# Kernel optimization log

Hardware: AMD Instinct MI355X
Metric: run time of the kernel (lower is better)

## Reference

```python
import jax, jax.numpy as jnp
import numpy as np

NODE = 100   # sensors per graph
BATCH = 64
DIM = 128    # embed dim == gnn out channels
IN_DIM = 5
TOPK = 30
INTER = 256  # out_layer hidden
EPS = 1e-5   # BatchNorm eps
SLOPE = 0.2  # leaky relu negative slope


def setup_inputs() -> dict:
    key = jax.random.key(0)
    ks = jax.random.split(key, 16)
    d = {
        "x": jax.random.normal(ks[0], (BATCH * NODE, IN_DIM), jnp.float32),
        "emb": jax.random.normal(ks[1], (NODE, DIM), jnp.float32) * 0.1,
        "w_lin": jax.random.normal(ks[2], (DIM, IN_DIM), jnp.float32) * (1.0 / np.sqrt(IN_DIM)),
        "att_i": jax.random.normal(ks[3], (DIM,), jnp.float32) * (1.0 / np.sqrt(DIM)),
        "att_j": jax.random.normal(ks[4], (DIM,), jnp.float32) * (1.0 / np.sqrt(DIM)),
        "att_em_i": jax.random.normal(ks[5], (DIM,), jnp.float32) * (1.0 / np.sqrt(DIM)),
        "att_em_j": jax.random.normal(ks[6], (DIM,), jnp.float32) * (1.0 / np.sqrt(DIM)),
        "g_bias": jax.random.normal(ks[7], (DIM,), jnp.float32) * 0.02,
        "bn1_g": jnp.ones((DIM,), jnp.float32),
        "bn1_b": jnp.zeros((DIM,), jnp.float32),
        "bn2_g": jnp.ones((DIM,), jnp.float32),
        "bn2_b": jnp.zeros((DIM,), jnp.float32),
        "bn3_g": jnp.ones((INTER,), jnp.float32),
        "bn3_b": jnp.zeros((INTER,), jnp.float32),
        "w1": jax.random.normal(ks[8], (INTER, DIM), jnp.float32) * (1.0 / np.sqrt(DIM)),
        "b1": jnp.zeros((INTER,), jnp.float32),
        "w2": jax.random.normal(ks[9], (1, INTER), jnp.float32) * (1.0 / np.sqrt(INTER)),
        "b2": jnp.zeros((1,), jnp.float32),
        "topk": TOPK,
    }
    return d


def _bn(z, g, b, axes):
    # BatchNorm1d in training mode: biased batch stats per channel (last axis)
    mu = z.mean(axes, keepdims=True)
    var = z.var(axes, keepdims=True)
    return (z - mu) / jnp.sqrt(var + EPS) * g + b


def reference(x, emb, w_lin, att_i, att_j, att_em_i, att_em_j, g_bias,
              bn1_g, bn1_b, bn2_g, bn2_b, bn3_g, bn3_b, w1, b1, w2, b2, topk):
    n, d = emb.shape
    nb = x.shape[0]            # batch*node rows
    bsz = nb // n

    # --- learned graph from cosine similarity of (detached) embeddings ---
    w = jax.lax.stop_gradient(emb)
    nrm = jnp.linalg.norm(w, axis=-1)
    cos = (w @ w.T) / (nrm[:, None] * nrm[None, :])
    _, idx = jax.lax.top_k(cos, topk)              # [n, k] neighbors j per target i
    src = idx.reshape(-1)                          # gated_j (source)
    dst = jnp.repeat(jnp.arange(n), topk)          # gated_i (target)
    off = (jnp.arange(bsz) * n)[:, None]
    src_b = (src[None, :] + off).reshape(-1)       # [bsz*n*k]
    dst_b = (dst[None, :] + off).reshape(-1)

    # --- GraphLayer: lin + gather + edge attention + segment softmax + scatter-add ---
    h = x @ w_lin.T                                # [nb, d]
    x_i = h[dst_b]
    x_j = h[src_b]
    emb_i = emb[dst_b % n]                         # all_embeddings repeated per batch
    emb_j = emb[src_b % n]
    alpha = x_i @ att_i + emb_i @ att_em_i + x_j @ att_j + emb_j @ att_em_j  # [E]
    alpha = jnp.where(alpha > 0, alpha, SLOPE * alpha)
    # segment softmax keyed by target node
    m = jax.ops.segment_max(alpha, dst_b, num_segments=nb)
    a = jnp.exp(alpha - m[dst_b])
    s = jax.ops.segment_sum(a, dst_b, num_segments=nb)
    attw = a / (s[dst_b] + 1e-16)
    agg = jax.ops.segment_sum(x_j * attw[:, None], dst_b, num_segments=nb) + g_bias

    # GNNLayer: BN + ReLU
    y = jax.nn.relu(_bn(agg, bn1_g, bn1_b, 0))     # [nb, d]

    # --- GDN head ---
    x3 = y.reshape(bsz, n, d) * emb[None]          # mul with node embeddings
    x3 = jax.nn.relu(_bn(x3, bn2_g, bn2_b, (0, 1)))
    # OutLayer: Linear -> BN -> ReLU -> Linear
    o = x3 @ w1.T + b1                             # [bsz, n, INTER]
    o = jax.nn.relu(_bn(o, bn3_g, bn3_b, (0, 1)))
    o = o @ w2.T + b2                              # [bsz, n, 1]
    return o.reshape(-1, 1)
```

## Files before the change

kernel.cpp:

```cpp
#include <hip/hip_runtime.h>

#define NODE 100
#define BATCH 64
#define DIM 128
#define IN_DIM 5
#define TOPK 30
#define INTER 256
#define NB (BATCH*NODE)
#define EPS 1e-5f
#define SLOPE 0.2f
#define REP 32

#define OFF_AGG    0
#define OFF_X3     819200
#define OFF_O1     1638400
#define OFF_U      3276800
#define OFF_EI     3276816
#define OFF_EJ     3276928
#define OFF_STATA  3277056
#define OFF_STAT2  3278080
#define OFF_STAT3  3286272
#define ZERO_LEN   25600
#define OFF_IDX    3302656

__global__ __launch_bounds__(256) void k_front(
        const float* __restrict__ emb, const float* __restrict__ w_lin,
        const float* __restrict__ att_i, const float* __restrict__ att_j,
        const float* __restrict__ att_em_i, const float* __restrict__ att_em_j,
        float* __restrict__ ws, int* __restrict__ idx) {
    __shared__ float smem[12800 + 128];
    int b = blockIdx.x, t = threadIdx.x, w = t >> 6, l = t & 63;
    if (b < 25) {
        float* eT = smem;
        float* nsq = smem + 12800;
        for (int i = t; i < NODE*DIM; i += 256) {
            int node = i >> 7, d = i & 127;
            eT[d*NODE + node] = emb[i];
        }
        __syncthreads();
        if (t < NODE) {
            float s = 0.f;
            for (int d = 0; d < DIM; ++d) { float v = eT[d*NODE + t]; s += v*v; }
            nsq[t] = s;
        }
        __syncthreads();
        int i = b*4 + w;
        int j0 = l, j1 = l + 64;
        bool ok1 = (j1 < NODE);
        float d0 = 0.f, d1 = 0.f;
        for (int dd = 0; dd < DIM; ++dd) {
            float ei = eT[dd*NODE + i];
            d0 += ei * eT[dd*NODE + j0];
            if (ok1) d1 += ei * eT[dd*NODE + j1];
        }
        float sni = sqrtf(nsq[i]);
        float c0 = d0 / (sni * sqrtf(nsq[j0]));
        float c1 = ok1 ? d1 / (sni * sqrtf(nsq[j1])) : -INFINITY;
        for (int r = 0; r < TOPK; ++r) {
            float bv; int bi;
            if (c1 > c0) { bv = c1; bi = j1; } else { bv = c0; bi = j0; }
#pragma unroll
            for (int m = 32; m >= 1; m >>= 1) {
                float ov = __shfl_xor(bv, m, 64);
                int   oi = __shfl_xor(bi, m, 64);
                if (ov > bv || (ov == bv && oi < bi)) { bv = ov; bi = oi; }
            }
            if (l == 0) idx[i*TOPK + r] = bi;
            if (bi == j0) c0 = -INFINITY;
            if (bi == j1) c1 = -INFINITY;
        }
    } else if (b == 25) {
        float* Pi = smem;
        float* Pj = smem + 640;
        if (t < DIM) {
            float wi = att_i[t], wj = att_j[t];
#pragma unroll
            for (int c = 0; c < IN_DIM; ++c) {
                float wl = w_lin[t*IN_DIM + c];
                Pi[c*128 + t] = wl*wi;
                Pj[c*128 + t] = wl*wj;
            }
        }
        __syncthreads();
        if (t < 10) {
            int c = (t < 5) ? t : t - 5;
            const float* P = (t < 5) ? Pi : Pj;
            float s = 0.f;
            for (int k = 0; k < DIM; ++k) s += P[c*128 + k];
            ws[OFF_U + t] = s;
        }
        float a0 = att_em_i[l], a1 = att_em_i[l+64];
        float b0 = att_em_j[l], b1 = att_em_j[l+64];
        for (int n = w*25; n < w*25 + 25; ++n) {
            float v0 = emb[n*DIM + l], v1 = emb[n*DIM + l + 64];
            float pi = v0*a0 + v1*a1;
            float pj = v0*b0 + v1*b1;
#pragma unroll
            for (int m = 32; m >= 1; m >>= 1) {
                pi += __shfl_xor(pi, m, 64);
                pj += __shfl_xor(pj, m, 64);
            }
            if (l == 0) { ws[OFF_EI + n] = pi; ws[OFF_EJ + n] = pj; }
        }
    } else {
        for (int i = t; i < ZERO_LEN; i += 256) ws[OFF_STATA + i] = 0.f;
    }
}

__global__ __launch_bounds__(128) void k_agg(
        const float* __restrict__ x, const float* __restrict__ w_lin,
        const float* __restrict__ g_bias, const int* __restrict__ idx,
        float* __restrict__ ws) {
    __shared__ float xl[NODE*IN_DIM];
    __shared__ float sjl[NODE];
    __shared__ float ul[10];
    __shared__ int   idl[4*TOPK];
    __shared__ float psum[2][20];
    int g = blockIdx.x, t = threadIdx.x, w = t >> 6, l = t & 63;
    int batch = g / 25;
    int nb0 = (g % 25) * 4;
    float* agg = ws + OFF_AGG;
    for (int i = t; i < NODE*IN_DIM; i += 128) xl[i] = x[batch*NODE*IN_DIM + i];
    for (int i = t; i < 4*TOPK; i += 128) idl[i] = idx[nb0*TOPK + i];
    if (t < 10) ul[t] = ws[OFF_U + t];
    __syncthreads();
    if (t < NODE) {
        float s = ws[OFF_EJ + t];
#pragma unroll
        for (int c = 0; c < IN_DIM; ++c) s += xl[t*IN_DIM + c] * ul[5 + c];
        sjl[t] = s;
    }
    __syncthreads();
    float wl0[IN_DIM], wl1[IN_DIM];
#pragma unroll
    for (int c = 0; c < IN_DIM; ++c) {
        wl0[c] = w_lin[l*IN_DIM + c];
        wl1[c] = w_lin[(l+64)*IN_DIM + c];
    }
    float gb0 = g_bias[l], gb1 = g_bias[l+64];
    float S0=0,S1=0,S2=0,S3=0,S4=0;
    float M[15];
#pragma unroll
    for (int m = 0; m < 15; ++m) M[m] = 0.f;
    for (int lt = w; lt < 4; lt += 2) {
        int node = nb0 + lt;
        int tgt = batch*NODE + node;
        float si = ws[OFF_EI + node];
#pragma unroll
        for (int c = 0; c < IN_DIM; ++c) si += xl[node*IN_DIM + c] * ul[c];
        float mx = -INFINITY;
#pragma unroll
        for (int r = 0; r < TOPK; ++r) {
            int s = idl[lt*TOPK + r];
            float a = si + sjl[s];
            a = (a > 0.f) ? a : SLOPE*a;
            mx = fmaxf(mx, a);
        }
        float ssum = 0.f, x0=0,x1=0,x2=0,x3v=0,x4=0;
#pragma unroll
        for (int r = 0; r < TOPK; ++r) {
            int s = idl[lt*TOPK + r];
            float a = si + sjl[s];
            a = (a > 0.f) ? a : SLOPE*a;
            float e = expf(a - mx);
            ssum += e;
            const float* xr = &xl[s*IN_DIM];
            x0 += e*xr[0]; x1 += e*xr[1]; x2 += e*xr[2]; x3v += e*xr[3]; x4 += e*xr[4];
        }
        float inv = 1.f/(ssum + 1e-16f);
        float y0=x0*inv, y1=x1*inv, y2=x2*inv, y3=x3v*inv, y4=x4*inv;
        float o0 = y0*wl0[0]+y1*wl0[1]+y2*wl0[2]+y3*wl0[3]+y4*wl0[4] + gb0;
        float o1 = y0*wl1[0]+y1*wl1[1]+y2*wl1[2]+y3*wl1[3]+y4*wl1[4] + gb1;
        agg[tgt*DIM + l]      = o0;
        agg[tgt*DIM + l + 64] = o1;
        S0+=y0; S1+=y1; S2+=y2; S3+=y3; S4+=y4;
        M[0]+=y0*y0; M[1]+=y0*y1; M[2]+=y0*y2; M[3]+=y0*y3; M[4]+=y0*y4;
        M[5]+=y1*y1; M[6]+=y1*y2; M[7]+=y1*y3; M[8]+=y1*y4;
        M[9]+=y2*y2; M[10]+=y2*y3; M[11]+=y2*y4;
        M[12]+=y3*y3; M[13]+=y3*y4; M[14]+=y4*y4;
    }
    if (l == 0) {
        psum[w][0]=S0; psum[w][1]=S1; psum[w][2]=S2; psum[w][3]=S3; psum[w][4]=S4;
#pragma unroll
        for (int m = 0; m < 15; ++m) psum[w][5+m] = M[m];
    }
    __syncthreads();
    if (t < 20) {
        float p = psum[0][t] + psum[1][t];
        atomicAdd(&ws[OFF_STATA + (g & (REP-1))*32 + t], p);
    }
}

__global__ __launch_bounds__(256) void k_x3(
        const float* __restrict__ w_lin, const float* __restrict__ g_bias,
        const float* __restrict__ emb,
        const float* __restrict__ g1, const float* __restrict__ b1,
        float* __restrict__ ws) {
    __shared__ float A[20];
    __shared__ float pv[8][DIM], pq[8][DIM];
    int t = threadIdx.x;
    if (t < 20) {
        float s = 0.f;
#pragma unroll
        for (int r = 0; r < REP; ++r) s += ws[OFF_STATA + r*32 + t];
        A[t] = s;
    }
    __syncthreads();
    const float invn = 1.f/(float)NB;
    int i4 = blockIdx.x*256 + t;
    int c4 = (i4 & 31) * 4;
    int row = i4 >> 5;
    int node = row % NODE;
    const float* agg = ws + OFF_AGG;
    float4 av = ((const float4*)agg)[i4];
    float4 ev = *(const float4*)&emb[node*DIM + c4];
    float o[4];
#pragma unroll
    for (int q = 0; q < 4; ++q) {
        int c = c4 + q;
        float w0 = w_lin[c*IN_DIM+0], w1 = w_lin[c*IN_DIM+1], w2 = w_lin[c*IN_DIM+2],
              w3 = w_lin[c*IN_DIM+3], w4 = w_lin[c*IN_DIM+4];
        float Sv = A[0]*w0 + A[1]*w1 + A[2]*w2 + A[3]*w3 + A[4]*w4;
        float Q  = w0*w0*A[5] + w1*w1*A[10] + w2*w2*A[14] + w3*w3*A[17] + w4*w4*A[19]
                 + 2.f*(w0*w1*A[6] + w0*w2*A[7] + w0*w3*A[8] + w0*w4*A[9]
                      + w1*w2*A[11] + w1*w3*A[12] + w1*w4*A[13]
                      + w2*w3*A[15] + w2*w4*A[16] + w3*w4*A[18]);
        float mv = Sv*invn;
        float mu = mv + g_bias[c];
        float var = fmaxf(Q*invn - mv*mv, 0.f);
        float rs = rsqrtf(var + EPS);
        float val = (((const float*)&av)[q] - mu)*rs*g1[c] + b1[c];
        val = fmaxf(val, 0.f);
        o[q] = val * ((const float*)&ev)[q];
    }
    ((float4*)(ws + OFF_X3))[i4] = make_float4(o[0], o[1], o[2], o[3]);
    int lr = t >> 5;
    *(float4*)&pv[lr][c4] = make_float4(o[0], o[1], o[2], o[3]);
    *(float4*)&pq[lr][c4] = make_float4(o[0]*o[0], o[1]*o[1], o[2]*o[2], o[3]*o[3]);
    __syncthreads();
    if (t < DIM) {
        float s1 = 0.f, s2 = 0.f;
#pragma unroll
        for (int r = 0; r < 8; ++r) { s1 += pv[r][t]; s2 += pq[r][t]; }
        int rep = blockIdx.x & (REP-1);
        atomicAdd(&ws[OFF_STAT2 + rep*256 + t], s1);
        atomicAdd(&ws[OFF_STAT2 + rep*256 + DIM + t], s2);
    }
}

__global__ __launch_bounds__(256) void k_gemm1(
        const float* __restrict__ g2, const float* __restrict__ b2v,
        const float* __restrict__ w1, const float* __restrict__ b1v,
        float* __restrict__ ws) {
    __shared__ float aT[32][36];
    __shared__ float wT[32][260];
    __shared__ float ps[4][INTER], ps2[4][INTER];
    __shared__ float bn2raw[256], mu2l[DIM], rs2l[DIM];
    int tid = threadIdx.x;
    const float invn = 1.f/(float)NB;
    {
        float s = 0.f;
#pragma unroll
        for (int r = 0; r < REP; ++r) s += ws[OFF_STAT2 + r*256 + tid];
        bn2raw[tid] = s;
    }
    __syncthreads();
    if (tid < DIM) {
        float mu = bn2raw[tid]*invn;
        float var = fmaxf(bn2raw[DIM + tid]*invn - mu*mu, 0.f);
        mu2l[tid] = mu;
        rs2l[tid] = rsqrtf(var + EPS);
    }
    __syncthreads();
    const float* x3 = ws + OFF_X3;
    float* o1 = ws + OFF_O1;
    int r0 = blockIdx.x * 32;
    int cg = tid & 63;
    int rg = tid >> 6;
    float acc[8][4];
#pragma unroll
    for (int a = 0; a < 8; ++a)
#pragma unroll
        for (int b = 0; b < 4; ++b) acc[a][b] = 0.f;
    int kk = tid & 31;
    for (int k0 = 0; k0 < DIM; k0 += 32) {
        int k = k0 + kk;
        float mu = mu2l[k], rs = rs2l[k], gg = g2[k], bb = b2v[k];
#pragma unroll
        for (int j = 0; j < 4; ++j) {
            int row = (tid >> 5) + j*8;
            float v = (x3[(r0+row)*DIM + k] - mu)*rs*gg + bb;
            aT[row][kk] = fmaxf(v, 0.f);
        }
#pragma unroll
        for (int j = 0; j < 32; ++j) {
            int i = tid + j*256;
            int kk2 = i & 31, c = i >> 5;
            wT[kk2][c] = w1[c*DIM + k0 + kk2];
        }
        __syncthreads();
#pragma unroll
        for (int q4 = 0; q4 < 8; ++q4) {
            float4 av[8], wv[4];
#pragma unroll
            for (int rr = 0; rr < 8; ++rr)
                av[rr] = *(const float4*)&aT[rg*8+rr][q4*4];
#pragma unroll
            for (int q = 0; q < 4; ++q)
                wv[q] = *(const float4*)&wT[q4*4+q][cg*4];
#pragma unroll
            for (int rr = 0; rr < 8; ++rr) {
                acc[rr][0] += av[rr].x*wv[0].x + av[rr].y*wv[1].x + av[rr].z*wv[2].x + av[rr].w*wv[3].x;
                acc[rr][1] += av[rr].x*wv[0].y + av[rr].y*wv[1].y + av[rr].z*wv[2].y + av[rr].w*wv[3].y;
                acc[rr][2] += av[rr].x*wv[0].z + av[rr].y*wv[1].z + av[rr].z*wv[2].z + av[rr].w*wv[3].z;
                acc[rr][3] += av[rr].x*wv[0].w + av[rr].y*wv[1].w + av[rr].z*wv[2].w + av[rr].w*wv[3].w;
            }
        }
        __syncthreads();
    }
    int cbase = cg*4;
    float4 bv = *(const float4*)&b1v[cbase];
    float lv[4]  = {0.f,0.f,0.f,0.f};
    float lv2[4] = {0.f,0.f,0.f,0.f};
#pragma unroll
    for (int rr = 0; rr < 8; ++rr) {
        int row = r0 + rg*8 + rr;
        float o0 = acc[rr][0] + bv.x;
        float o1v = acc[rr][1] + bv.y;
        float o2 = acc[rr][2] + bv.z;
        float o3 = acc[rr][3] + bv.w;
        *(float4*)&o1[row*INTER + cbase] = make_float4(o0, o1v, o2, o3);
        lv[0]+=o0;  lv2[0]+=o0*o0;
        lv[1]+=o1v; lv2[1]+=o1v*o1v;
        lv[2]+=o2;  lv2[2]+=o2*o2;
        lv[3]+=o3;  lv2[3]+=o3*o3;
    }
    *(float4*)&ps[rg][cbase]  = make_float4(lv[0], lv[1], lv[2], lv[3]);
    *(float4*)&ps2[rg][cbase] = make_float4(lv2[0], lv2[1], lv2[2], lv2[3]);
    __syncthreads();
    if (tid < INTER) {
        float s1 = ps[0][tid] + ps[1][tid] + ps[2][tid] + ps[3][tid];
        float s2 = ps2[0][tid] + ps2[1][tid] + ps2[2][tid] + ps2[3][tid];
        int rep = blockIdx.x & (REP-1);
        atomicAdd(&ws[OFF_STAT3 + rep*512 + tid], s1);
        atomicAdd(&ws[OFF_STAT3 + rep*512 + INTER + tid], s2);
    }
}

__global__ __launch_bounds__(512) void k_out(
        const float* __restrict__ g3, const float* __restrict__ b3,
        const float* __restrict__ w2, const float* __restrict__ b2s,
        const float* __restrict__ ws, float* __restrict__ out) {
    __shared__ float raw[512], mu3l[INTER], rs3l[INTER];
    int t = threadIdx.x, w = t >> 6, l = t & 63;
    const float invn = 1.f/(float)NB;
    {
        float s = 0.f;
#pragma unroll
        for (int r = 0; r < REP; ++r) s += ws[OFF_STAT3 + r*512 + t];
        raw[t] = s;
    }
    __syncthreads();
    if (t < INTER) {
        float mu = raw[t]*invn;
        float var = fmaxf(raw[INTER + t]*invn - mu*mu, 0.f);
        mu3l[t] = mu;
        rs3l[t] = rsqrtf(var + EPS);
    }
    __syncthreads();
    int row = blockIdx.x*8 + w;
    const float* o1 = ws + OFF_O1;
    float4 v = *(const float4*)&o1[row*INTER + l*4];
    float s = 0.f;
#pragma unroll
    for (int q = 0; q < 4; ++q) {
        int c = l*4 + q;
        float val = (((const float*)&v)[q] - mu3l[c])*rs3l[c]*g3[c] + b3[c];
        val = fmaxf(val, 0.f);
        s += val * w2[c];
    }
#pragma unroll
    for (int m = 32; m >= 1; m >>= 1) s += __shfl_xor(s, m, 64);
    if (l == 0) out[row] = s + b2s[0];
}

extern "C" void kernel_launch(void* const* d_in, const int* in_sizes, int n_in,
                              void* d_out, int out_size, void* d_ws, size_t ws_size,
                              hipStream_t stream) {
    const float* x        = (const float*)d_in[0];
    const float* emb      = (const float*)d_in[1];
    const float* w_lin    = (const float*)d_in[2];
    const float* att_i    = (const float*)d_in[3];
    const float* att_j    = (const float*)d_in[4];
    const float* att_em_i = (const float*)d_in[5];
    const float* att_em_j = (const float*)d_in[6];
    const float* g_bias   = (const float*)d_in[7];
    const float* bn1_g    = (const float*)d_in[8];
    const float* bn1_b    = (const float*)d_in[9];
    const float* bn2_g    = (const float*)d_in[10];
    const float* bn2_b    = (const float*)d_in[11];
    const float* bn3_g    = (const float*)d_in[12];
    const float* bn3_b    = (const float*)d_in[13];
    const float* w1       = (const float*)d_in[14];
    const float* b1       = (const float*)d_in[15];
    const float* w2       = (const float*)d_in[16];
    const float* b2       = (const float*)d_in[17];
    float* out = (float*)d_out;
    float* ws  = (float*)d_ws;
    int*   idx = (int*)(ws + OFF_IDX);

    k_front<<<27, 256, 0, stream>>>(emb, w_lin, att_i, att_j, att_em_i, att_em_j, ws, idx);
    k_agg<<<1600, 128, 0, stream>>>(x, w_lin, g_bias, idx, ws);
    k_x3<<<NB*DIM/4/256, 256, 0, stream>>>(w_lin, g_bias, emb, bn1_g, bn1_b, ws);
    k_gemm1<<<NB/32, 256, 0, stream>>>(bn2_g, bn2_b, w1, b1, ws);
    k_out<<<NB/8, 512, 0, stream>>>(bn3_g, bn3_b, w2, b2, ws, out);
}
```

Baseline: 165.8 us.

## Fuse all stages into one persistent kernel with software grid barriers

Replaces five kernel launches with one persistent kernel of 256 blocks that separates the stages with atomic-counter grid barriers. The stats workspace and barrier counters are now zeroed with a memset. Each stage loops over its work items block-strided, and BN2 partial stats are accumulated in registers across iterations before the atomics. This removes per-launch overhead and gaps between kernels, at the cost of limited parallelism per stage. It also depends on all 256 blocks being co-resident, or the barriers deadlock.

```diff
diff --git a/kernel.cpp b/kernel.cpp
--- a/kernel.cpp
+++ b/kernel.cpp
@@ -10,6 +10,7 @@
 #define EPS 1e-5f
 #define SLOPE 0.2f
 #define REP 32
+#define NBLK 256
 
 #define OFF_AGG    0
 #define OFF_X3     819200
@@ -20,18 +21,42 @@
 #define OFF_STATA  3277056
 #define OFF_STAT2  3278080
 #define OFF_STAT3  3286272
-#define ZERO_LEN   25600
-#define OFF_IDX    3302656
-
-__global__ __launch_bounds__(256) void k_front(
-        const float* __restrict__ emb, const float* __restrict__ w_lin,
+#define OFF_BAR    3302656
+#define OFF_IDX    3302672
+#define ZERO_BYTES ((OFF_BAR + 16 - OFF_STATA) * 4)
+
+__device__ __forceinline__ void gbar(int* cnt) {
+    __syncthreads();
+    if (threadIdx.x == 0) {
+        __threadfence();
+        __hip_atomic_fetch_add(cnt, 1, __ATOMIC_ACQ_REL, __HIP_MEMORY_SCOPE_AGENT);
+        while (__hip_atomic_load(cnt, __ATOMIC_ACQUIRE, __HIP_MEMORY_SCOPE_AGENT) < NBLK) {
+            __builtin_amdgcn_s_sleep(1);
+        }
+        __threadfence();
+    }
+    __syncthreads();
+}
+
+__global__ __launch_bounds__(256, 1) void k_fused(
+        const float* __restrict__ x, const float* __restrict__ emb,
+        const float* __restrict__ w_lin,
         const float* __restrict__ att_i, const float* __restrict__ att_j,
         const float* __restrict__ att_em_i, const float* __restrict__ att_em_j,
-        float* __restrict__ ws, int* __restrict__ idx) {
-    __shared__ float smem[12800 + 128];
-    int b = blockIdx.x, t = threadIdx.x, w = t >> 6, l = t & 63;
+        const float* __restrict__ g_bias,
+        const float* __restrict__ g1, const float* __restrict__ b1,
+        const float* __restrict__ g2, const float* __restrict__ b2v,
+        const float* __restrict__ g3, const float* __restrict__ b3,
+        const float* __restrict__ w1, const float* __restrict__ b1v,
+        const float* __restrict__ w2, const float* __restrict__ b2s,
+        float* __restrict__ ws, int* __restrict__ idx, float* __restrict__ out) {
+    __shared__ __align__(16) float smem[12928];
+    int* bar = (int*)(ws + OFF_BAR);
+    const int b = blockIdx.x, t = threadIdx.x, w = t >> 6, l = t & 63;
+    const float invn = 1.f/(float)NB;
+
     if (b < 25) {
-        float* eT = smem;
+        float* eT  = smem;
         float* nsq = smem + 12800;
         for (int i = t; i < NODE*DIM; i += 256) {
             int node = i >> 7, d = i & 127;
@@ -90,11 +115,11 @@
             ws[OFF_U + t] = s;
         }
         float a0 = att_em_i[l], a1 = att_em_i[l+64];
-        float b0 = att_em_j[l], b1 = att_em_j[l+64];
+        float b0 = att_em_j[l], b1v_ = att_em_j[l+64];
         for (int n = w*25; n < w*25 + 25; ++n) {
             float v0 = emb[n*DIM + l], v1 = emb[n*DIM + l + 64];
             float pi = v0*a0 + v1*a1;
-            float pj = v0*b0 + v1*b1;
+            float pj = v0*b0 + v1*b1v_;
 #pragma unroll
             for (int m = 32; m >= 1; m >>= 1) {
                 pi += __shfl_xor(pi, m, 64);
@@ -102,286 +127,303 @@
             }
             if (l == 0) { ws[OFF_EI + n] = pi; ws[OFF_EJ + n] = pj; }
         }
-    } else {
-        for (int i = t; i < ZERO_LEN; i += 256) ws[OFF_STATA + i] = 0.f;
-    }
-}
-
-__global__ __launch_bounds__(128) void k_agg(
-        const float* __restrict__ x, const float* __restrict__ w_lin,
-        const float* __restrict__ g_bias, const int* __restrict__ idx,
-        float* __restrict__ ws) {
-    __shared__ float xl[NODE*IN_DIM];
-    __shared__ float sjl[NODE];
-    __shared__ float ul[10];
-    __shared__ int   idl[4*TOPK];
-    __shared__ float psum[2][20];
-    int g = blockIdx.x, t = threadIdx.x, w = t >> 6, l = t & 63;
-    int batch = g / 25;
-    int nb0 = (g % 25) * 4;
-    float* agg = ws + OFF_AGG;
-    for (int i = t; i < NODE*IN_DIM; i += 128) xl[i] = x[batch*NODE*IN_DIM + i];
-    for (int i = t; i < 4*TOPK; i += 128) idl[i] = idx[nb0*TOPK + i];
-    if (t < 10) ul[t] = ws[OFF_U + t];
-    __syncthreads();
-    if (t < NODE) {
-        float s = ws[OFF_EJ + t];
-#pragma unroll
-        for (int c = 0; c < IN_DIM; ++c) s += xl[t*IN_DIM + c] * ul[5 + c];
-        sjl[t] = s;
-    }
-    __syncthreads();
-    float wl0[IN_DIM], wl1[IN_DIM];
-#pragma unroll
-    for (int c = 0; c < IN_DIM; ++c) {
-        wl0[c] = w_lin[l*IN_DIM + c];
-        wl1[c] = w_lin[(l+64)*IN_DIM + c];
-    }
-    float gb0 = g_bias[l], gb1 = g_bias[l+64];
-    float S0=0,S1=0,S2=0,S3=0,S4=0;
-    float M[15];
-#pragma unroll
-    for (int m = 0; m < 15; ++m) M[m] = 0.f;
-    for (int lt = w; lt < 4; lt += 2) {
-        int node = nb0 + lt;
-        int tgt = batch*NODE + node;
-        float si = ws[OFF_EI + node];
-#pragma unroll
-        for (int c = 0; c < IN_DIM; ++c) si += xl[node*IN_DIM + c] * ul[c];
-        float mx = -INFINITY;
-#pragma unroll
-        for (int r = 0; r < TOPK; ++r) {
-            int s = idl[lt*TOPK + r];
-            float a = si + sjl[s];
-            a = (a > 0.f) ? a : SLOPE*a;
-            mx = fmaxf(mx, a);
-        }
-        float ssum = 0.f, x0=0,x1=0,x2=0,x3v=0,x4=0;
-#pragma unroll
-        for (int r = 0; r < TOPK; ++r) {
-            int s = idl[lt*TOPK + r];
-            float a = si + sjl[s];
-            a = (a > 0.f) ? a : SLOPE*a;
-            float e = expf(a - mx);
-            ssum += e;
-            const float* xr = &xl[s*IN_DIM];
-            x0 += e*xr[0]; x1 += e*xr[1]; x2 += e*xr[2]; x3v += e*xr[3]; x4 += e*xr[4];
-        }
-        float inv = 1.f/(ssum + 1e-16f);
-        float y0=x0*inv, y1=x1*inv, y2=x2*inv, y3=x3v*inv, y4=x4*inv;
-        float o0 = y0*wl0[0]+y1*wl0[1]+y2*wl0[2]+y3*wl0[3]+y4*wl0[4] + gb0;
-        float o1 = y0*wl1[0]+y1*wl1[1]+y2*wl1[2]+y3*wl1[3]+y4*wl1[4] + gb1;
-        agg[tgt*DIM + l]      = o0;
-        agg[tgt*DIM + l + 64] = o1;
-        S0+=y0; S1+=y1; S2+=y2; S3+=y3; S4+=y4;
-        M[0]+=y0*y0; M[1]+=y0*y1; M[2]+=y0*y2; M[3]+=y0*y3; M[4]+=y0*y4;
-        M[5]+=y1*y1; M[6]+=y1*y2; M[7]+=y1*y3; M[8]+=y1*y4;
-        M[9]+=y2*y2; M[10]+=y2*y3; M[11]+=y2*y4;
-        M[12]+=y3*y3; M[13]+=y3*y4; M[14]+=y4*y4;
-    }
-    if (l == 0) {
-        psum[w][0]=S0; psum[w][1]=S1; psum[w][2]=S2; psum[w][3]=S3; psum[w][4]=S4;
-#pragma unroll
-        for (int m = 0; m < 15; ++m) psum[w][5+m] = M[m];
-    }
-    __syncthreads();
-    if (t < 20) {
-        float p = psum[0][t] + psum[1][t];
-        atomicAdd(&ws[OFF_STATA + (g & (REP-1))*32 + t], p);
-    }
-}
-
-__global__ __launch_bounds__(256) void k_x3(
-        const float* __restrict__ w_lin, const float* __restrict__ g_bias,
-        const float* __restrict__ emb,
-        const float* __restrict__ g1, const float* __restrict__ b1,
-        float* __restrict__ ws) {
-    __shared__ float A[20];
-    __shared__ float pv[8][DIM], pq[8][DIM];
-    int t = threadIdx.x;
-    if (t < 20) {
-        float s = 0.f;
-#pragma unroll
-        for (int r = 0; r < REP; ++r) s += ws[OFF_STATA + r*32 + t];
-        A[t] = s;
-    }
-    __syncthreads();
-    const float invn = 1.f/(float)NB;
-    int i4 = blockIdx.x*256 + t;
-    int c4 = (i4 & 31) * 4;
-    int row = i4 >> 5;
-    int node = row % NODE;
-    const float* agg = ws + OFF_AGG;
-    float4 av = ((const float4*)agg)[i4];
-    float4 ev = *(const float4*)&emb[node*DIM + c4];
-    float o[4];
-#pragma unroll
-    for (int q = 0; q < 4; ++q) {
-        int c = c4 + q;
-        float w0 = w_lin[c*IN_DIM+0], w1 = w_lin[c*IN_DIM+1], w2 = w_lin[c*IN_DIM+2],
-              w3 = w_lin[c*IN_DIM+3], w4 = w_lin[c*IN_DIM+4];
-        float Sv = A[0]*w0 + A[1]*w1 + A[2]*w2 + A[3]*w3 + A[4]*w4;
-        float Q  = w0*w0*A[5] + w1*w1*A[10] + w2*w2*A[14] + w3*w3*A[17] + w4*w4*A[19]
-                 + 2.f*(w0*w1*A[6] + w0*w2*A[7] + w0*w3*A[8] + w0*w4*A[9]
-                      + w1*w2*A[11] + w1*w3*A[12] + w1*w4*A[13]
-                      + w2*w3*A[15] + w2*w4*A[16] + w3*w4*A[18]);
-        float mv = Sv*invn;
-        float mu = mv + g_bias[c];
-        float var = fmaxf(Q*invn - mv*mv, 0.f);
-        float rs = rsqrtf(var + EPS);
-        float val = (((const float*)&av)[q] - mu)*rs*g1[c] + b1[c];
-        val = fmaxf(val, 0.f);
-        o[q] = val * ((const float*)&ev)[q];
-    }
-    ((float4*)(ws + OFF_X3))[i4] = make_float4(o[0], o[1], o[2], o[3]);
-    int lr = t >> 5;
-    *(float4*)&pv[lr][c4] = make_float4(o[0], o[1], o[2], o[3]);
-    *(float4*)&pq[lr][c4] = make_float4(o[0]*o[0], o[1]*o[1], o[2]*o[2], o[3]*o[3]);
-    __syncthreads();
-    if (t < DIM) {
-        float s1 = 0.f, s2 = 0.f;
-#pragma unroll
-        for (int r = 0; r < 8; ++r) { s1 += pv[r][t]; s2 += pq[r][t]; }
-        int rep = blockIdx.x & (REP-1);
-        atomicAdd(&ws[OFF_STAT2 + rep*256 + t], s1);
-        atomicAdd(&ws[OFF_STAT2 + rep*256 + DIM + t], s2);
-    }
-}
-
-__global__ __launch_bounds__(256) void k_gemm1(
-        const float* __restrict__ g2, const float* __restrict__ b2v,
-        const float* __restrict__ w1, const float* __restrict__ b1v,
-        float* __restrict__ ws) {
-    __shared__ float aT[32][36];
-    __shared__ float wT[32][260];
-    __shared__ float ps[4][INTER], ps2[4][INTER];
-    __shared__ float bn2raw[256], mu2l[DIM], rs2l[DIM];
-    int tid = threadIdx.x;
-    const float invn = 1.f/(float)NB;
+    }
+    gbar(&bar[0]);
+
     {
-        float s = 0.f;
-#pragma unroll
-        for (int r = 0; r < REP; ++r) s += ws[OFF_STAT2 + r*256 + tid];
-        bn2raw[tid] = s;
-    }
-    __syncthreads();
-    if (tid < DIM) {
-        float mu = bn2raw[tid]*invn;
-        float var = fmaxf(bn2raw[DIM + tid]*invn - mu*mu, 0.f);
-        mu2l[tid] = mu;
-        rs2l[tid] = rsqrtf(var + EPS);
-    }
-    __syncthreads();
-    const float* x3 = ws + OFF_X3;
-    float* o1 = ws + OFF_O1;
-    int r0 = blockIdx.x * 32;
-    int cg = tid & 63;
-    int rg = tid >> 6;
-    float acc[8][4];
-#pragma unroll
-    for (int a = 0; a < 8; ++a)
-#pragma unroll
-        for (int b = 0; b < 4; ++b) acc[a][b] = 0.f;
-    int kk = tid & 31;
-    for (int k0 = 0; k0 < DIM; k0 += 32) {
-        int k = k0 + kk;
-        float mu = mu2l[k], rs = rs2l[k], gg = g2[k], bb = b2v[k];
-#pragma unroll
-        for (int j = 0; j < 4; ++j) {
-            int row = (tid >> 5) + j*8;
-            float v = (x3[(r0+row)*DIM + k] - mu)*rs*gg + bb;
-            aT[row][kk] = fmaxf(v, 0.f);
-        }
-#pragma unroll
-        for (int j = 0; j < 32; ++j) {
-            int i = tid + j*256;
-            int kk2 = i & 31, c = i >> 5;
-            wT[kk2][c] = w1[c*DIM + k0 + kk2];
-        }
-        __syncthreads();
-#pragma unroll
-        for (int q4 = 0; q4 < 8; ++q4) {
-            float4 av[8], wv[4];
-#pragma unroll
-            for (int rr = 0; rr < 8; ++rr)
-                av[rr] = *(const float4*)&aT[rg*8+rr][q4*4];
-#pragma unroll
-            for (int q = 0; q < 4; ++q)
-                wv[q] = *(const float4*)&wT[q4*4+q][cg*4];
-#pragma unroll
-            for (int rr = 0; rr < 8; ++rr) {
-                acc[rr][0] += av[rr].x*wv[0].x + av[rr].y*wv[1].x + av[rr].z*wv[2].x + av[rr].w*wv[3].x;
-                acc[rr][1] += av[rr].x*wv[0].y + av[rr].y*wv[1].y + av[rr].z*wv[2].y + av[rr].w*wv[3].y;
-                acc[rr][2] += av[rr].x*wv[0].z + av[rr].y*wv[1].z + av[rr].z*wv[2].z + av[rr].w*wv[3].z;
-                acc[rr][3] += av[rr].x*wv[0].w + av[rr].y*wv[1].w + av[rr].z*wv[2].w + av[rr].w*wv[3].w;
-            }
-        }
-        __syncthreads();
-    }
-    int cbase = cg*4;
-    float4 bv = *(const float4*)&b1v[cbase];
-    float lv[4]  = {0.f,0.f,0.f,0.f};
-    float lv2[4] = {0.f,0.f,0.f,0.f};
-#pragma unroll
-    for (int rr = 0; rr < 8; ++rr) {
-        int row = r0 + rg*8 + rr;
-        float o0 = acc[rr][0] + bv.x;
-        float o1v = acc[rr][1] + bv.y;
-        float o2 = acc[rr][2] + bv.z;
-        float o3 = acc[rr][3] + bv.w;
-        *(float4*)&o1[row*INTER + cbase] = make_float4(o0, o1v, o2, o3);
-        lv[0]+=o0;  lv2[0]+=o0*o0;
-        lv[1]+=o1v; lv2[1]+=o1v*o1v;
-        lv[2]+=o2;  lv2[2]+=o2*o2;
-        lv[3]+=o3;  lv2[3]+=o3*o3;
-    }
-    *(float4*)&ps[rg][cbase]  = make_float4(lv[0], lv[1], lv[2], lv[3]);
-    *(float4*)&ps2[rg][cbase] = make_float4(lv2[0], lv2[1], lv2[2], lv2[3]);
-    __syncthreads();
-    if (tid < INTER) {
-        float s1 = ps[0][tid] + ps[1][tid] + ps[2][tid] + ps[3][tid];
-        float s2 = ps2[0][tid] + ps2[1][tid] + ps2[2][tid] + ps2[3][tid];
-        int rep = blockIdx.x & (REP-1);
-        atomicAdd(&ws[OFF_STAT3 + rep*512 + tid], s1);
-        atomicAdd(&ws[OFF_STAT3 + rep*512 + INTER + tid], s2);
-    }
-}
-
-__global__ __launch_bounds__(512) void k_out(
-        const float* __restrict__ g3, const float* __restrict__ b3,
-        const float* __restrict__ w2, const float* __restrict__ b2s,
-        const float* __restrict__ ws, float* __restrict__ out) {
-    __shared__ float raw[512], mu3l[INTER], rs3l[INTER];
-    int t = threadIdx.x, w = t >> 6, l = t & 63;
-    const float invn = 1.f/(float)NB;
+        float* ul   = smem;
+        float* xl   = smem + 16;
+        float* sjl  = smem + 1016;
+        int*   idl  = (int*)(smem + 1216);
+        float* psum = smem + 1456;
+        float* agg  = ws + OFF_AGG;
+        if (t < 10) ul[t] = ws[OFF_U + t];
+        float wl0[IN_DIM], wl1[IN_DIM];
+#pragma unroll
+        for (int c = 0; c < IN_DIM; ++c) {
+            wl0[c] = w_lin[l*IN_DIM + c];
+            wl1[c] = w_lin[(l+64)*IN_DIM + c];
+        }
+        float gb0 = g_bias[l], gb1 = g_bias[l+64];
+        float S0=0,S1=0,S2=0,S3=0,S4=0;
+        float M[15];
+#pragma unroll
+        for (int m = 0; m < 15; ++m) M[m] = 0.f;
+        int half = t >> 7, ht = t & 127, hw = (t >> 6) & 1;
+        for (int v = b; v < 800; v += NBLK) {
+            __syncthreads();
+            int item = v*2 + half;
+            int batch = item / 25;
+            int nb0 = (item % 25) * 4;
+            for (int i = ht; i < NODE*IN_DIM; i += 128) xl[half*500 + i] = x[batch*NODE*IN_DIM + i];
+            for (int i = ht; i < 4*TOPK; i += 128) idl[half*120 + i] = idx[nb0*TOPK + i];
+            __syncthreads();
+            if (ht < NODE) {
+                float s = ws[OFF_EJ + ht];
+#pragma unroll
+                for (int c = 0; c < IN_DIM; ++c) s += xl[half*500 + ht*IN_DIM + c] * ul[5 + c];
+                sjl[half*100 + ht] = s;
+            }
+            __syncthreads();
+            for (int lt = hw; lt < 4; lt += 2) {
+                int node = nb0 + lt;
+                int tgt = batch*NODE + node;
+                float si = ws[OFF_EI + node];
+#pragma unroll
+                for (int c = 0; c < IN_DIM; ++c) si += xl[half*500 + node*IN_DIM + c] * ul[c];
+                float mx = -INFINITY;
+#pragma unroll
+                for (int r = 0; r < TOPK; ++r) {
+                    int s = idl[half*120 + lt*TOPK + r];
+                    float a = si + sjl[half*100 + s];
+                    a = (a > 0.f) ? a : SLOPE*a;
+                    mx = fmaxf(mx, a);
+                }
+                float ssum = 0.f, x0=0,x1=0,x2=0,x3v=0,x4=0;
+#pragma unroll
+                for (int r = 0; r < TOPK; ++r) {
+                    int s = idl[half*120 + lt*TOPK + r];
+                    float a = si + sjl[half*100 + s];
+                    a = (a > 0.f) ? a : SLOPE*a;
+                    float e = expf(a - mx);
+                    ssum += e;
+                    const float* xr = &xl[half*500 + s*IN_DIM];
+                    x0 += e*xr[0]; x1 += e*xr[1]; x2 += e*xr[2]; x3v += e*xr[3]; x4 += e*xr[4];
+                }
+                float inv = 1.f/(ssum + 1e-16f);
+                float y0=x0*inv, y1=x1*inv, y2=x2*inv, y3=x3v*inv, y4=x4*inv;
+                float o0 = y0*wl0[0]+y1*wl0[1]+y2*wl0[2]+y3*wl0[3]+y4*wl0[4] + gb0;
+                float o1 = y0*wl1[0]+y1*wl1[1]+y2*wl1[2]+y3*wl1[3]+y4*wl1[4] + gb1;
+                agg[tgt*DIM + l]      = o0;
+                agg[tgt*DIM + l + 64] = o1;
+                S0+=y0; S1+=y1; S2+=y2; S3+=y3; S4+=y4;
+                M[0]+=y0*y0; M[1]+=y0*y1; M[2]+=y0*y2; M[3]+=y0*y3; M[4]+=y0*y4;
+                M[5]+=y1*y1; M[6]+=y1*y2; M[7]+=y1*y3; M[8]+=y1*y4;
+                M[9]+=y2*y2; M[10]+=y2*y3; M[11]+=y2*y4;
+                M[12]+=y3*y3; M[13]+=y3*y4; M[14]+=y4*y4;
+            }
+        }
+        __syncthreads();
+        if (l == 0) {
+            psum[w*20+0]=S0; psum[w*20+1]=S1; psum[w*20+2]=S2; psum[w*20+3]=S3; psum[w*20+4]=S4;
+#pragma unroll
+            for (int m = 0; m < 15; ++m) psum[w*20+5+m] = M[m];
+        }
+        __syncthreads();
+        if (t < 20) {
+            float p = psum[t] + psum[20+t] + psum[40+t] + psum[60+t];
+            atomicAdd(&ws[OFF_STATA + (b & (REP-1))*32 + t], p);
+        }
+    }
+    gbar(&bar[1]);
+
     {
-        float s = 0.f;
-#pragma unroll
-        for (int r = 0; r < REP; ++r) s += ws[OFF_STAT3 + r*512 + t];
-        raw[t] = s;
-    }
-    __syncthreads();
-    if (t < INTER) {
-        float mu = raw[t]*invn;
-        float var = fmaxf(raw[INTER + t]*invn - mu*mu, 0.f);
-        mu3l[t] = mu;
-        rs3l[t] = rsqrtf(var + EPS);
-    }
-    __syncthreads();
-    int row = blockIdx.x*8 + w;
-    const float* o1 = ws + OFF_O1;
-    float4 v = *(const float4*)&o1[row*INTER + l*4];
-    float s = 0.f;
-#pragma unroll
-    for (int q = 0; q < 4; ++q) {
-        int c = l*4 + q;
-        float val = (((const float*)&v)[q] - mu3l[c])*rs3l[c]*g3[c] + b3[c];
-        val = fmaxf(val, 0.f);
-        s += val * w2[c];
-    }
-#pragma unroll
-    for (int m = 32; m >= 1; m >>= 1) s += __shfl_xor(s, m, 64);
-    if (l == 0) out[row] = s + b2s[0];
+        float* A  = smem;
+        float* pv = smem + 32;
+        float* pq = smem + 1056;
+        if (t < 20) {
+            float s = 0.f;
+#pragma unroll
+            for (int r = 0; r < REP; ++r) s += ws[OFF_STATA + r*32 + t];
+            A[t] = s;
+        }
+        __syncthreads();
+        int cq = (t & 31) * 4;
+        float muq[4], rsg[4], bq[4];
+#pragma unroll
+        for (int q = 0; q < 4; ++q) {
+            int c = cq + q;
+            float w0 = w_lin[c*IN_DIM+0], w1v = w_lin[c*IN_DIM+1], w2v = w_lin[c*IN_DIM+2],
+                  w3 = w_lin[c*IN_DIM+3], w4 = w_lin[c*IN_DIM+4];
+            float Sv = A[0]*w0 + A[1]*w1v + A[2]*w2v + A[3]*w3 + A[4]*w4;
+            float Q  = w0*w0*A[5] + w1v*w1v*A[10] + w2v*w2v*A[14] + w3*w3*A[17] + w4*w4*A[19]
+                     + 2.f*(w0*w1v*A[6] + w0*w2v*A[7] + w0*w3*A[8] + w0*w4*A[9]
+                          + w1v*w2v*A[11] + w1v*w3*A[12] + w1v*w4*A[13]
+                          + w2v*w3*A[15] + w2v*w4*A[16] + w3*w4*A[18]);
+            float mv = Sv*invn;
+            float mu = mv + g_bias[c];
+            float var = fmaxf(Q*invn - mv*mv, 0.f);
+            float rs = rsqrtf(var + EPS);
+            muq[q] = mu; rsg[q] = rs*g1[c]; bq[q] = b1[c];
+        }
+        const float4* agg4 = (const float4*)(ws + OFF_AGG);
+        const float4* emb4 = (const float4*)emb;
+        float4* x34 = (float4*)(ws + OFF_X3);
+        float a1[4] = {0,0,0,0}, a2[4] = {0,0,0,0};
+        for (int v = b; v < 800; v += NBLK) {
+            int i4 = v*256 + t;
+            int row = i4 >> 5;
+            int node = row % NODE;
+            float4 av = agg4[i4];
+            float4 ev = emb4[node*32 + (t & 31)];
+            float o[4];
+#pragma unroll
+            for (int q = 0; q < 4; ++q) {
+                float val = (((const float*)&av)[q] - muq[q])*rsg[q] + bq[q];
+                val = fmaxf(val, 0.f);
+                o[q] = val * ((const float*)&ev)[q];
+                a1[q] += o[q];
+                a2[q] += o[q]*o[q];
+            }
+            x34[i4] = make_float4(o[0], o[1], o[2], o[3]);
+        }
+        int g = t >> 5;
+        *(float4*)&pv[g*128 + cq] = make_float4(a1[0], a1[1], a1[2], a1[3]);
+        *(float4*)&pq[g*128 + cq] = make_float4(a2[0], a2[1], a2[2], a2[3]);
+        __syncthreads();
+        if (t < DIM) {
+            float s1 = 0.f, s2 = 0.f;
+#pragma unroll
+            for (int r = 0; r < 8; ++r) { s1 += pv[r*128 + t]; s2 += pq[r*128 + t]; }
+            int rep = b & (REP-1);
+            atomicAdd(&ws[OFF_STAT2 + rep*256 + t], s1);
+            atomicAdd(&ws[OFF_STAT2 + rep*256 + DIM + t], s2);
+        }
+    }
+    gbar(&bar[2]);
+
+    if (b < 200) {
+        float* aT     = smem;
+        float* wT     = smem + 1152;
+        float* ps     = smem + 9472;
+        float* ps2    = smem + 10496;
+        float* bn2raw = smem + 11520;
+        float* mu2l   = smem + 11776;
+        float* rs2l   = smem + 11904;
+        {
+            float s = 0.f;
+#pragma unroll
+            for (int r = 0; r < REP; ++r) s += ws[OFF_STAT2 + r*256 + t];
+            bn2raw[t] = s;
+        }
+        __syncthreads();
+        if (t < DIM) {
+            float mu = bn2raw[t]*invn;
+            float var = fmaxf(bn2raw[DIM + t]*invn - mu*mu, 0.f);
+            mu2l[t] = mu;
+            rs2l[t] = rsqrtf(var + EPS);
+        }
+        __syncthreads();
+        const float* x3 = ws + OFF_X3;
+        float* o1 = ws + OFF_O1;
+        int r0 = b * 32;
+        int cg = t & 63;
+        int rg = t >> 6;
+        float acc[8][4];
+#pragma unroll
+        for (int a = 0; a < 8; ++a)
+#pragma unroll
+            for (int q = 0; q < 4; ++q) acc[a][q] = 0.f;
+        int kk = t & 31;
+        for (int k0 = 0; k0 < DIM; k0 += 32) {
+            int k = k0 + kk;
+            float mu = mu2l[k], rs = rs2l[k], gg = g2[k], bb = b2v[k];
+#pragma unroll
+            for (int j = 0; j < 4; ++j) {
+                int row = (t >> 5) + j*8;
+                float v = (x3[(r0+row)*DIM + k] - mu)*rs*gg + bb;
+                aT[row*36 + kk] = fmaxf(v, 0.f);
+            }
+#pragma unroll
+            for (int j = 0; j < 32; ++j) {
+                int i = t + j*256;
+                int kk2 = i & 31, c = i >> 5;
+                wT[kk2*260 + c] = w1[c*DIM + k0 + kk2];
+            }
+            __syncthreads();
+#pragma unroll
+            for (int q4 = 0; q4 < 8; ++q4) {
+                float4 av[8], wv[4];
+#pragma unroll
+                for (int rr = 0; rr < 8; ++rr)
+                    av[rr] = *(const float4*)&aT[(rg*8+rr)*36 + q4*4];
+#pragma unroll
+                for (int q = 0; q < 4; ++q)
+                    wv[q] = *(const float4*)&wT[(q4*4+q)*260 + cg*4];
+#pragma unroll
+                for (int rr = 0; rr < 8; ++rr) {
+                    acc[rr][0] += av[rr].x*wv[0].x + av[rr].y*wv[1].x + av[rr].z*wv[2].x + av[rr].w*wv[3].x;
+                    acc[rr][1] += av[rr].x*wv[0].y + av[rr].y*wv[1].y + av[rr].z*wv[2].y + av[rr].w*wv[3].y;
+                    acc[rr][2] += av[rr].x*wv[0].z + av[rr].y*wv[1].z + av[rr].z*wv[2].z + av[rr].w*wv[3].z;
+                    acc[rr][3] += av[rr].x*wv[0].w + av[rr].y*wv[1].w + av[rr].z*wv[2].w + av[rr].w*wv[3].w;
+                }
+            }
+            __syncthreads();
+        }
+        int cbase = cg*4;
+        float4 bv = *(const float4*)&b1v[cbase];
+        float lv[4]  = {0,0,0,0};
+        float lv2[4] = {0,0,0,0};
+#pragma unroll
+        for (int rr = 0; rr < 8; ++rr) {
+            int row = r0 + rg*8 + rr;
+            float o0 = acc[rr][0] + bv.x;
+            float o1v = acc[rr][1] + bv.y;
+            float o2 = acc[rr][2] + bv.z;
+            float o3 = acc[rr][3] + bv.w;
+            *(float4*)&o1[row*INTER + cbase] = make_float4(o0, o1v, o2, o3);
+            lv[0]+=o0;  lv2[0]+=o0*o0;
+            lv[1]+=o1v; lv2[1]+=o1v*o1v;
+            lv[2]+=o2;  lv2[2]+=o2*o2;
+            lv[3]+=o3;  lv2[3]+=o3*o3;
+        }
+        *(float4*)&ps[rg*256 + cbase]  = make_float4(lv[0], lv[1], lv[2], lv[3]);
+        *(float4*)&ps2[rg*256 + cbase] = make_float4(lv2[0], lv2[1], lv2[2], lv2[3]);
+        __syncthreads();
+        if (t < INTER) {
+            float s1 = ps[t] + ps[256+t] + ps[512+t] + ps[768+t];
+            float s2 = ps2[t] + ps2[256+t] + ps2[512+t] + ps2[768+t];
+            int rep = b & (REP-1);
+            atomicAdd(&ws[OFF_STAT3 + rep*512 + t], s1);
+            atomicAdd(&ws[OFF_STAT3 + rep*512 + INTER + t], s2);
+        }
+    }
+    gbar(&bar[3]);
+
+    {
+        float* raw  = smem;
+        float* mu3l = smem + 512;
+        float* rs3l = smem + 768;
+        for (int tt = t; tt < 512; tt += 256) {
+            float s = 0.f;
+#pragma unroll
+            for (int r = 0; r < REP; ++r) s += ws[OFF_STAT3 + r*512 + tt];
+            raw[tt] = s;
+        }
+        __syncthreads();
+        {
+            float mu = raw[t]*invn;
+            float var = fmaxf(raw[256 + t]*invn - mu*mu, 0.f);
+            mu3l[t] = mu;
+            rs3l[t] = rsqrtf(var + EPS);
+        }
+        __syncthreads();
+        float m3[4], rg3[4], b3q[4], w2q[4];
+#pragma unroll
+        for (int q = 0; q < 4; ++q) {
+            int c = l*4 + q;
+            m3[q] = mu3l[c];
+            rg3[q] = rs3l[c]*g3[c];
+            b3q[q] = b3[c];
+            w2q[q] = w2[c];
+        }
+        float bias2 = b2s[0];
+        const float4* o14 = (const float4*)(ws + OFF_O1);
+        for (int v = b; v < 1600; v += NBLK) {
+            int row = v*4 + w;
+            float4 vv = o14[row*64 + l];
+            float s = 0.f;
+#pragma unroll
+            for (int q = 0; q < 4; ++q) {
+                float val = (((const float*)&vv)[q] - m3[q])*rg3[q] + b3q[q];
+                val = fmaxf(val, 0.f);
+                s += val * w2q[q];
+            }
+#pragma unroll
+            for (int m = 32; m >= 1; m >>= 1) s += __shfl_xor(s, m, 64);
+            if (l == 0) out[row] = s + bias2;
+        }
+    }
 }
 
 extern "C" void kernel_launch(void* const* d_in, const int* in_sizes, int n_in,
@@ -409,9 +451,9 @@
     float* ws  = (float*)d_ws;
     int*   idx = (int*)(ws + OFF_IDX);
 
-    k_front<<<27, 256, 0, stream>>>(emb, w_lin, att_i, att_j, att_em_i, att_em_j, ws, idx);
-    k_agg<<<1600, 128, 0, stream>>>(x, w_lin, g_bias, idx, ws);
-    k_x3<<<NB*DIM/4/256, 256, 0, stream>>>(w_lin, g_bias, emb, bn1_g, bn1_b, ws);
-    k_gemm1<<<NB/32, 256, 0, stream>>>(bn2_g, bn2_b, w1, b1, ws);
-    k_out<<<NB/8, 512, 0, stream>>>(bn3_g, bn3_b, w2, b2, ws, out);
+    hipMemsetAsync((void*)(ws + OFF_STATA), 0, ZERO_BYTES, stream);
+
+    k_fused<<<NBLK, 256, 0, stream>>>(x, emb, w_lin, att_i, att_j, att_em_i,
+                                      att_em_j, g_bias, bn1_g, bn1_b, bn2_g, bn2_b,
+                                      bn3_g, bn3_b, w1, b1, w2, b2, ws, idx, out);
 }
```

Result: slower. 297.7 us (+79.6%).
